# Performance work log

Hardware: AMD Instinct MI355X
Metric: run time of the kernel (lower is better)

The kernel has to match this reference:

```python
import jax, jax.numpy as jnp
import numpy as np

MIN_LOGITS_VALUE = -2.3819763e+38
MAX_WAVELENGTH = 10000


def _apply_rope(inputs, positions):
    # inputs: [b, t, n, h]; positions: [b, t]. RoPE on first half of h.
    x_rope, x = jnp.split(inputs, 2, axis=-1)
    pos = positions[:, :, None, None].astype(jnp.float32)  # [b, t, 1, 1]
    freq_exponents = 2.0 * jnp.arange(x_rope.shape[-1] // 2) / x_rope.shape[-1]
    inv_freq = 1.0 / (MAX_WAVELENGTH ** freq_exponents)
    sinusoid = pos * inv_freq  # [b, t, 1, h/2]
    sin = jnp.sin(sinusoid).astype(inputs.dtype)
    cos = jnp.cos(sinusoid).astype(inputs.dtype)
    first, second = jnp.split(x_rope, 2, axis=-1)
    return jnp.concatenate(
        [first * cos - second * sin, second * cos + first * sin, x], axis=-1)


def _forward_pass_mask(segment_pos, window_size):
    # segment_pos: [b, t]; 0 marks a segment start.
    segment_ids = jnp.cumsum(segment_pos == 0, axis=-1)  # [b, t]
    t = segment_pos.shape[-1]
    positions = jnp.arange(t)
    same_segment = segment_ids[:, :, None] == segment_ids[:, None, :]
    causal = positions[:, None] >= positions[None, :]
    window = positions[:, None] <= positions[None, :] + window_size
    return same_segment & (causal & window)[None]  # [b, t, t]


def setup_inputs() -> dict:
    key = jax.random.key(0)
    ks = jax.random.split(key, 6)
    B, T, W, N = 2, 2048, 2048, 16
    H = W // N
    x = jax.random.normal(ks[0], (B, T, W), jnp.float32)
    sc = 1.0 / np.sqrt(W).astype(np.float32)
    w_q = jax.random.normal(ks[1], (W, W), jnp.float32) * sc
    w_k = jax.random.normal(ks[2], (W, H), jnp.float32) * sc
    w_v = jax.random.normal(ks[3], (W, H), jnp.float32) * sc
    w_out = jax.random.normal(ks[4], (W, W), jnp.float32) * sc
    b_out = jnp.zeros((W,), jnp.float32)
    segment_pos = jnp.tile(jnp.arange(T, dtype=jnp.int32)[None], (B, 1))
    return {"x": x, "w_q": w_q, "w_k": w_k, "w_v": w_v, "w_out": w_out,
            "b_out": b_out, "segment_pos": segment_pos,
            "num_heads": N, "window_size": 1024}


def reference(x, w_q, w_k, w_v, w_out, b_out, segment_pos, num_heads, window_size):
    b, t, width = x.shape
    head_dim = width // num_heads
    # Projections: MQA -> keys/values are single-head [b, t, head_dim].
    q = (x @ w_q).reshape(b, t, num_heads, head_dim)
    k = (x @ w_k)[:, :, None, :]  # [b, t, 1, h]
    v = x @ w_v                   # [b, t, h]
    q = _apply_rope(q, segment_pos)
    k = _apply_rope(k, segment_pos)[:, :, 0]  # [b, t, h]
    logits = jnp.einsum('btnh,bsh->bnts', q, k) * (head_dim ** -0.5)
    mask = _forward_pass_mask(segment_pos, window_size)  # [b, t, t]
    masked = jnp.where(mask[:, None], logits, MIN_LOGITS_VALUE).astype(jnp.float32)
    probs = jax.nn.softmax(masked, axis=-1).astype(x.dtype)
    encoded = jnp.einsum('bnts,bsh->btnh', probs, v).reshape(b, t, width)
    return encoded @ w_out + b_out
```

## Files before the change

kernel.cpp:

```cpp
#include <hip/hip_runtime.h>
#include <hip/hip_bf16.h>
#include <stdint.h>

typedef __attribute__((ext_vector_type(8))) short short8;
typedef __attribute__((ext_vector_type(4))) float f32x4;

__device__ __forceinline__ float bf2f(short u) {
  return __uint_as_float(((unsigned)(unsigned short)u) << 16);
}
__device__ __forceinline__ short f2bf(float f) {
  unsigned x = __float_as_uint(f);
  unsigned r = (x + 0x7fffu + ((x >> 16) & 1u)) >> 16;
  return (short)r;
}

__device__ __forceinline__ void gload_lds16(const short* g, short* l) {
  __builtin_amdgcn_global_load_lds(
      (const __attribute__((address_space(1))) void*)g,
      (__attribute__((address_space(3))) void*)l, 16, 0, 0);
}

__global__ void cast_x_bf16(const float* __restrict__ in, short* __restrict__ out, int n8) {
  int i = blockIdx.x * blockDim.x + threadIdx.x;
  if (i >= n8) return;
  const float4* p = (const float4*)in + (size_t)i * 2;
  float4 a = p[0], b = p[1];
  short8 o;
  o[0] = f2bf(a.x); o[1] = f2bf(a.y); o[2] = f2bf(a.z); o[3] = f2bf(a.w);
  o[4] = f2bf(b.x); o[5] = f2bf(b.y); o[6] = f2bf(b.z); o[7] = f2bf(b.w);
  *((short8*)out + i) = o;
}

__global__ void transpose_cast(const float* __restrict__ in, int R, int C,
                               short* __restrict__ out, int row_off, int ldo) {
  __shared__ float tile[32][33];
  int c0 = blockIdx.x * 32, r0 = blockIdx.y * 32;
  int tx = threadIdx.x, ty = threadIdx.y;
#pragma unroll
  for (int i = 0; i < 4; ++i)
    tile[ty + i * 8][tx] = in[(size_t)(r0 + ty + i * 8) * C + (c0 + tx)];
  __syncthreads();
#pragma unroll
  for (int i = 0; i < 4; ++i)
    out[(size_t)(row_off + c0 + ty + i * 8) * ldo + (r0 + tx)] =
        f2bf(tile[tx][ty + i * 8]);
}

__global__ void transpose_v(const short* __restrict__ qkv, short* __restrict__ vT,
                            int T, int LD, int vcol) {
  __shared__ short tile[32][33];
  int t0 = blockIdx.x * 32, h0 = blockIdx.y * 32, b = blockIdx.z;
  int tx = threadIdx.x, ty = threadIdx.y;
#pragma unroll
  for (int i = 0; i < 4; ++i)
    tile[ty + i * 8][tx] = qkv[((size_t)b * T + t0 + ty + i * 8) * LD + vcol + h0 + tx];
  __syncthreads();
#pragma unroll
  for (int i = 0; i < 4; ++i)
    vT[((size_t)b * 128 + h0 + ty + i * 8) * T + t0 + tx] = tile[tx][ty + i * 8];
}

template <int OUT_F32>
__global__ __launch_bounds__(512, 2)
void gemm256(const short* __restrict__ A, const short* __restrict__ Bt,
             int M, int N, int K, int ldc,
             short* __restrict__ outb, float* __restrict__ outf,
             const float* __restrict__ bias) {
  __shared__ short As[2][256 * 64];
  __shared__ short Bs[2][256 * 64];
  const int tid = threadIdx.x, lane = tid & 63, w = tid >> 6;
  const int wm = w >> 2, wn = w & 3;
  const int l15 = lane & 15, l4 = lane >> 4;
  const int m0 = blockIdx.y * 256, n0 = blockIdx.x * 256;
  const int sw = (l15 & 7) << 4;
  const int NT = K / 64;

  f32x4 acc[8][4] = {};
  short8 a[4][2], b[4][2];

  auto stage = [&](short* dst, const short* src, int base0, int k0) {
#pragma unroll
    for (int i = 0; i < 4; ++i) {
      int chunk = i * 8 + w;
      int r = chunk * 8 + (lane >> 3);
      int cs = ((lane & 7) ^ ((lane >> 3) & 7)) * 8;
      gload_lds16(src + (size_t)(base0 + r) * K + k0 + cs, dst + chunk * 512);
    }
  };

  auto rdA = [&](const short* buf, int mi, int kk) -> short8 {
    int row = wm * 128 + mi * 16 + l15;
    int byt = row * 128 + ((kk * 64 + l4 * 16) ^ sw);
    return *(const short8*)((const char*)buf + byt);
  };
  auto rdB = [&](const short* buf, int ni, int kk) -> short8 {
    int row = wn * 64 + ni * 16 + l15;
    int byt = row * 128 + ((kk * 64 + l4 * 16) ^ sw);
    return *(const short8*)((const char*)buf + byt);
  };

  stage(As[0], A, m0, 0);
  stage(Bs[0], Bt, n0, 0);
  asm volatile("s_waitcnt vmcnt(0)" ::: "memory");
  __builtin_amdgcn_s_barrier();

  for (int t = 0; t < NT; ++t) {
    const int bf = t & 1, nb = bf ^ 1;
    const bool pre = (t + 1 < NT);
    const short* Ab = As[bf];
    const short* Bb = Bs[bf];

#pragma unroll
    for (int mg = 0; mg < 4; ++mg) { a[mg][0] = rdA(Ab, mg, 0); a[mg][1] = rdA(Ab, mg, 1); }
#pragma unroll
    for (int ng = 0; ng < 2; ++ng) { b[ng][0] = rdB(Bb, ng, 0); b[ng][1] = rdB(Bb, ng, 1); }
    if (pre) stage(As[nb], A, m0, (t + 1) * 64);
    __builtin_amdgcn_s_barrier();
    __builtin_amdgcn_s_setprio(1);
#pragma unroll
    for (int mg = 0; mg < 4; ++mg)
#pragma unroll
      for (int ng = 0; ng < 2; ++ng) {
        acc[mg][ng] = __builtin_amdgcn_mfma_f32_16x16x32_bf16(a[mg][0], b[ng][0], acc[mg][ng], 0, 0, 0);
        acc[mg][ng] = __builtin_amdgcn_mfma_f32_16x16x32_bf16(a[mg][1], b[ng][1], acc[mg][ng], 0, 0, 0);
      }
    __builtin_amdgcn_s_setprio(0);
    __builtin_amdgcn_s_barrier();

#pragma unroll
    for (int ng = 2; ng < 4; ++ng) { b[ng][0] = rdB(Bb, ng, 0); b[ng][1] = rdB(Bb, ng, 1); }
    if (pre) stage(Bs[nb], Bt, n0, (t + 1) * 64);
    __builtin_amdgcn_s_barrier();
    __builtin_amdgcn_s_setprio(1);
#pragma unroll
    for (int mg = 0; mg < 4; ++mg)
#pragma unroll
      for (int ng = 2; ng < 4; ++ng) {
        acc[mg][ng] = __builtin_amdgcn_mfma_f32_16x16x32_bf16(a[mg][0], b[ng][0], acc[mg][ng], 0, 0, 0);
        acc[mg][ng] = __builtin_amdgcn_mfma_f32_16x16x32_bf16(a[mg][1], b[ng][1], acc[mg][ng], 0, 0, 0);
      }
    __builtin_amdgcn_s_setprio(0);
    __builtin_amdgcn_s_barrier();

#pragma unroll
    for (int mg = 0; mg < 4; ++mg) { a[mg][0] = rdA(Ab, mg + 4, 0); a[mg][1] = rdA(Ab, mg + 4, 1); }
    __builtin_amdgcn_s_barrier();
    __builtin_amdgcn_s_setprio(1);
#pragma unroll
    for (int mg = 0; mg < 4; ++mg)
#pragma unroll
      for (int ng = 0; ng < 2; ++ng) {
        acc[mg + 4][ng] = __builtin_amdgcn_mfma_f32_16x16x32_bf16(a[mg][0], b[ng][0], acc[mg + 4][ng], 0, 0, 0);
        acc[mg + 4][ng] = __builtin_amdgcn_mfma_f32_16x16x32_bf16(a[mg][1], b[ng][1], acc[mg + 4][ng], 0, 0, 0);
      }
    __builtin_amdgcn_s_setprio(0);
    __builtin_amdgcn_s_barrier();

    __builtin_amdgcn_s_setprio(1);
#pragma unroll
    for (int mg = 0; mg < 4; ++mg)
#pragma unroll
      for (int ng = 2; ng < 4; ++ng) {
        acc[mg + 4][ng] = __builtin_amdgcn_mfma_f32_16x16x32_bf16(a[mg][0], b[ng][0], acc[mg + 4][ng], 0, 0, 0);
        acc[mg + 4][ng] = __builtin_amdgcn_mfma_f32_16x16x32_bf16(a[mg][1], b[ng][1], acc[mg + 4][ng], 0, 0, 0);
      }
    __builtin_amdgcn_s_setprio(0);
    asm volatile("s_waitcnt vmcnt(0)" ::: "memory");
    __builtin_amdgcn_s_barrier();
  }

#pragma unroll
  for (int mi = 0; mi < 8; ++mi)
#pragma unroll
    for (int ni = 0; ni < 4; ++ni)
#pragma unroll
      for (int r = 0; r < 4; ++r) {
        int row = m0 + wm * 128 + mi * 16 + l4 * 4 + r;
        int col = n0 + wn * 64 + ni * 16 + l15;
        if (OUT_F32)
          outf[(size_t)row * ldc + col] = acc[mi][ni][r] + bias[col];
        else
          outb[(size_t)row * ldc + col] = f2bf(acc[mi][ni][r]);
      }
}

__global__ void rope_kernel(short* __restrict__ qkv, const int* __restrict__ segpos,
                            int nheads, int hd, int ld) {
  const int row = blockIdx.x;
  const float pos = (float)segpos[row];
  short* base = qkv + (size_t)row * ld;
  const int quarter = hd >> 2;
  const int npairs_q = nheads * quarter;
  const int total = npairs_q + quarter;
  for (int p = threadIdx.x; p < total; p += blockDim.x) {
    int i, off;
    if (p < npairs_q) { off = (p >> 5) * hd; i = p & 31; }
    else              { off = nheads * hd;  i = p - npairs_q; }
    float ang = pos * exp2f(-(float)i * (13.287712379549449f / (float)quarter));
    float s, c;
    sincosf(ang, &s, &c);
    float a = bf2f(base[off + i]);
    float b = bf2f(base[off + quarter + i]);
    base[off + i]           = f2bf(a * c - b * s);
    base[off + quarter + i] = f2bf(b * c + a * s);
  }
}

__global__ __launch_bounds__(512)
void attn_kernel(const short* __restrict__ qkv, const short* __restrict__ vT,
                 short* __restrict__ enc,
                 const int* __restrict__ wsz_p, int T, int nheads, int nqt, int bhc) {
  const int window = wsz_p[0];
  const int i = blockIdx.x;
  const int qt = nqt - 1 - (i / bhc);
  const int bh = i % bhc;
  const int b = bh / nheads, n = bh % nheads;
  const int tid = threadIdx.x, lane = tid & 63, w = tid >> 6;
  const int l15 = lane & 15, l4 = lane >> 4;
  const int q0 = qt * 128;
  const size_t rowbase = (size_t)b * T;
  const int LD = nheads * 128 + 256;
  const int kcol = nheads * 128;
  const float CC = 0.08838834764831845f * 1.4426950408889634f;

  __shared__ short Ks[64 * 128];
  __shared__ short Vt[128 * 64];
  __shared__ short Pl[8][16 * 72];

  short8 qf[4];
  {
    const short* qptr = qkv + (rowbase + q0 + w * 16 + l15) * LD + n * 128 + l4 * 8;
#pragma unroll
    for (int kk = 0; kk < 4; ++kk) qf[kk] = *(const short8*)(qptr + kk * 32);
  }
  f32x4 o[8] = {};
  float mrow[4], lrow[4];
#pragma unroll
  for (int r = 0; r < 4; ++r) { mrow[r] = -1e30f; lrow[r] = 0.f; }

  const int tmin = q0 + w * 16, tmax = tmin + 15;
  int st_lo = q0 - window; if (st_lo < 0) st_lo = 0; st_lo >>= 6;
  const int st_hi = (q0 + 127) >> 6;

  short8 kreg[2], vreg[2];
  auto load_tile = [&](int s0) {
#pragma unroll
    for (int it = 0; it < 2; ++it) {
      int c = it * 512 + tid;
      kreg[it] = *(const short8*)(qkv + (rowbase + s0 + (c >> 4)) * (size_t)LD + kcol + (c & 15) * 8);
      vreg[it] = *(const short8*)(vT + ((size_t)b * 128 + (c >> 3)) * T + s0 + (c & 7) * 8);
    }
  };
  auto store_tile = [&]() {
#pragma unroll
    for (int it = 0; it < 2; ++it) {
      int c = it * 512 + tid;
      int r = c >> 4;
      *(short8*)((char*)Ks + ((r * 256 + (c & 15) * 16) ^ ((r & 7) << 4))) = kreg[it];
      int h = c >> 3;
      *(short8*)((char*)Vt + ((h * 128 + (c & 7) * 16) ^ ((h & 7) << 4))) = vreg[it];
    }
  };

  load_tile(st_lo * 64);
  store_tile();
  __syncthreads();

  for (int st = st_lo; st <= st_hi; ++st) {
    const int s0 = st * 64;
    const bool more = (st < st_hi);
    if (more) load_tile(s0 + 64);

    const bool active = (s0 <= tmax) && (tmin <= s0 + 63 + window);
    if (active) {
      f32x4 sacc[4];
      __builtin_amdgcn_s_setprio(1);
#pragma unroll
      for (int si = 0; si < 4; ++si) {
        f32x4 acc = {};
        int srow = si * 16 + l15;
#pragma unroll
        for (int kk = 0; kk < 4; ++kk) {
          int byt = (srow * 256 + (kk * 32 + l4 * 8) * 2) ^ ((srow & 7) << 4);
          short8 kf = *(const short8*)((const char*)Ks + byt);
          acc = __builtin_amdgcn_mfma_f32_16x16x32_bf16(qf[kk], kf, acc, 0, 0, 0);
        }
        sacc[si] = acc;
      }
      __builtin_amdgcn_s_setprio(0);

      const int trow0 = q0 + w * 16 + l4 * 4;
      const bool full = (s0 + 63 <= tmin) && (tmax <= s0 + window);
      float mt[4];
      if (full) {
#pragma unroll
        for (int r = 0; r < 4; ++r)
          mt[r] = fmaxf(fmaxf(sacc[0][r], sacc[1][r]), fmaxf(sacc[2][r], sacc[3][r]));
      } else {
#pragma unroll
        for (int r = 0; r < 4; ++r) mt[r] = -1e30f;
#pragma unroll
        for (int si = 0; si < 4; ++si) {
          int s = s0 + si * 16 + l15;
#pragma unroll
          for (int r = 0; r < 4; ++r) {
            int t = trow0 + r;
            float v = (s <= t && t <= s + window) ? sacc[si][r] : -1e30f;
            sacc[si][r] = v;
            mt[r] = fmaxf(mt[r], v);
          }
        }
      }
#pragma unroll
      for (int r = 0; r < 4; ++r)
#pragma unroll
        for (int off = 1; off < 16; off <<= 1)
          mt[r] = fmaxf(mt[r], __shfl_xor(mt[r], off));

      bool dfr = true;
#pragma unroll
      for (int r = 0; r < 4; ++r) dfr = dfr && ((mt[r] - mrow[r]) * CC <= 8.0f);
      const bool defer = __all(dfr);
      float fac[4];
      if (!defer) {
#pragma unroll
        for (int r = 0; r < 4; ++r) {
          float mnew = fmaxf(mrow[r], mt[r]);
          fac[r] = exp2f((mrow[r] - mnew) * CC);
          mrow[r] = mnew;
        }
      }
      float psum[4];
#pragma unroll
      for (int r = 0; r < 4; ++r) psum[r] = 0.f;
#pragma unroll
      for (int si = 0; si < 4; ++si)
#pragma unroll
        for (int r = 0; r < 4; ++r) {
          float p = exp2f((sacc[si][r] - mrow[r]) * CC);
          psum[r] += p;
          Pl[w][(l4 * 4 + r) * 72 + si * 16 + l15] = f2bf(p);
        }
#pragma unroll
      for (int r = 0; r < 4; ++r) {
#pragma unroll
        for (int off = 1; off < 16; off <<= 1)
          psum[r] += __shfl_xor(psum[r], off);
        if (!defer) lrow[r] = lrow[r] * fac[r] + psum[r];
        else        lrow[r] += psum[r];
      }
      if (!defer) {
#pragma unroll
        for (int nt = 0; nt < 8; ++nt)
#pragma unroll
          for (int r = 0; r < 4; ++r) o[nt][r] *= fac[r];
      }

      __builtin_amdgcn_s_setprio(1);
#pragma unroll
      for (int kk = 0; kk < 2; ++kk) {
        short8 pf = *(const short8*)(&Pl[w][l15 * 72 + kk * 32 + l4 * 8]);
#pragma unroll
        for (int nt = 0; nt < 8; ++nt) {
          int h = nt * 16 + l15;
          int vb = (h * 128 + kk * 64 + l4 * 16) ^ ((h & 7) << 4);
          short8 vf = *(const short8*)((const char*)Vt + vb);
          o[nt] = __builtin_amdgcn_mfma_f32_16x16x32_bf16(pf, vf, o[nt], 0, 0, 0);
        }
      }
      __builtin_amdgcn_s_setprio(0);
    }
    __syncthreads();
    if (more) store_tile();
    __syncthreads();
  }

#pragma unroll
  for (int nt = 0; nt < 8; ++nt)
#pragma unroll
    for (int r = 0; r < 4; ++r) {
      size_t row = rowbase + q0 + w * 16 + l4 * 4 + r;
      int col = n * 128 + nt * 16 + l15;
      enc[row * (size_t)(nheads * 128) + col] = f2bf(o[nt][r] / lrow[r]);
    }
}

extern "C" void kernel_launch(void* const* d_in, const int* in_sizes, int n_in,
                              void* d_out, int out_size, void* d_ws, size_t ws_size,
                              hipStream_t stream) {
  const float* x     = (const float*)d_in[0];
  const float* w_q   = (const float*)d_in[1];
  const float* w_k   = (const float*)d_in[2];
  const float* w_v   = (const float*)d_in[3];
  const float* w_out = (const float*)d_in[4];
  const float* b_out = (const float*)d_in[5];
  const int* segpos  = (const int*)d_in[6];
  const int* wsz     = (const int*)d_in[8];
  float* out = (float*)d_out;

  const int BT = in_sizes[6];
  const int W  = in_sizes[5];
  const int H  = in_sizes[2] / W;
  const int NH = W / H;
  const int T  = 2048;
  const int B  = BT / T;
  const int NQKV = W + 2 * H;

  char* ws = (char*)d_ws;
  short* xb    = (short*)ws;
  short* wqkvT = (short*)(ws + (size_t)BT * W * 2);
  short* woutT = (short*)(ws + (size_t)(BT * W + NQKV * W) * 2);
  short* qkv   = (short*)(ws + (size_t)(BT * W + NQKV * W + W * W) * 2);
  short* vTp   = wqkvT;
  short* enc   = xb;

  int n8 = BT * W / 8;
  cast_x_bf16<<<(n8 + 255) / 256, 256, 0, stream>>>(x, xb, n8);

  dim3 tb(32, 8);
  transpose_cast<<<dim3(W / 32, W / 32), tb, 0, stream>>>(w_q, W, W, wqkvT, 0, W);
  transpose_cast<<<dim3(H / 32, W / 32), tb, 0, stream>>>(w_k, W, H, wqkvT, W, W);
  transpose_cast<<<dim3(H / 32, W / 32), tb, 0, stream>>>(w_v, W, H, wqkvT, W + H, W);
  transpose_cast<<<dim3(W / 32, W / 32), tb, 0, stream>>>(w_out, W, W, woutT, 0, W);

  gemm256<0><<<dim3(NQKV / 256, BT / 256), 512, 0, stream>>>(
      xb, wqkvT, BT, NQKV, W, NQKV, qkv, nullptr, nullptr);

  rope_kernel<<<BT, 256, 0, stream>>>(qkv, segpos, NH, H, NQKV);

  transpose_v<<<dim3(T / 32, H / 32, B), tb, 0, stream>>>(qkv, vTp, T, NQKV, NH * H + H);

  const int nqt = T / 128;
  const int bhc = B * NH;
  attn_kernel<<<nqt * bhc, 512, 0, stream>>>(qkv, vTp, enc, wsz, T, NH, nqt, bhc);

  gemm256<1><<<dim3(W / 256, BT / 256), 512, 0, stream>>>(
      enc, woutT, BT, W, W, W, nullptr, out, b_out);
}
```

Measured before the change: 359.0 us.

## Replace double-buffered GEMM with four-slot K=32 ring pipeline

Rewrites the bf16 GEMM main loop to use a four-slot shared-memory ring of K=32 tiles, prefetching two steps ahead with partial vmcnt waits and a single barrier per iteration. It also changes the LDS swizzle to a 4-chunk XOR pattern. The aim is to cut the many barriers per K-step and hide global-load latency better. In exchange there are twice as many loop iterations, smaller MFMA batches per barrier, and a new swizzle that may cause LDS bank conflicts. The ring also relies on waitcnt accounting being correct for the global_load_lds ops.

After: 403.8 us. +12.5%, slower.

```diff
diff --git a/kernel.cpp b/kernel.cpp
--- a/kernel.cpp
+++ b/kernel.cpp
@@ -62,110 +62,62 @@
 
 template <int OUT_F32>
 __global__ __launch_bounds__(512, 2)
-void gemm256(const short* __restrict__ A, const short* __restrict__ Bt,
-             int M, int N, int K, int ldc,
-             short* __restrict__ outb, float* __restrict__ outf,
-             const float* __restrict__ bias) {
-  __shared__ short As[2][256 * 64];
-  __shared__ short Bs[2][256 * 64];
+void gemm_ring(const short* __restrict__ A, const short* __restrict__ Bt,
+               int M, int N, int K, int ldc,
+               short* __restrict__ outb, float* __restrict__ outf,
+               const float* __restrict__ bias) {
+  __shared__ short As[4][256 * 32];
+  __shared__ short Bs[4][256 * 32];
   const int tid = threadIdx.x, lane = tid & 63, w = tid >> 6;
   const int wm = w >> 2, wn = w & 3;
   const int l15 = lane & 15, l4 = lane >> 4;
   const int m0 = blockIdx.y * 256, n0 = blockIdx.x * 256;
-  const int sw = (l15 & 7) << 4;
-  const int NT = K / 64;
+  const int NT = K / 32;
+  const int cswz = (l4 ^ ((l15 >> 1) & 3)) * 8;
 
   f32x4 acc[8][4] = {};
-  short8 a[4][2], b[4][2];
-
-  auto stage = [&](short* dst, const short* src, int base0, int k0) {
-#pragma unroll
-    for (int i = 0; i < 4; ++i) {
-      int chunk = i * 8 + w;
-      int r = chunk * 8 + (lane >> 3);
-      int cs = ((lane & 7) ^ ((lane >> 3) & 7)) * 8;
-      gload_lds16(src + (size_t)(base0 + r) * K + k0 + cs, dst + chunk * 512);
-    }
-  };
-
-  auto rdA = [&](const short* buf, int mi, int kk) -> short8 {
-    int row = wm * 128 + mi * 16 + l15;
-    int byt = row * 128 + ((kk * 64 + l4 * 16) ^ sw);
-    return *(const short8*)((const char*)buf + byt);
-  };
-  auto rdB = [&](const short* buf, int ni, int kk) -> short8 {
-    int row = wn * 64 + ni * 16 + l15;
-    int byt = row * 128 + ((kk * 64 + l4 * 16) ^ sw);
-    return *(const short8*)((const char*)buf + byt);
+
+  auto stage = [&](short* dst, const short* src, int base0, int kt) {
+#pragma unroll
+    for (int i = 0; i < 2; ++i) {
+      int ci = tid + 512 * i;
+      int r = ci >> 2, s = ci & 3;
+      int gs = s ^ ((r >> 1) & 3);
+      gload_lds16(src + (size_t)(base0 + r) * K + kt * 32 + gs * 8, dst + ci * 8);
+    }
   };
 
   stage(As[0], A, m0, 0);
   stage(Bs[0], Bt, n0, 0);
-  asm volatile("s_waitcnt vmcnt(0)" ::: "memory");
+  stage(As[1], A, m0, 1);
+  stage(Bs[1], Bt, n0, 1);
+  asm volatile("s_waitcnt vmcnt(4)" ::: "memory");
   __builtin_amdgcn_s_barrier();
 
+#pragma unroll 4
   for (int t = 0; t < NT; ++t) {
-    const int bf = t & 1, nb = bf ^ 1;
-    const bool pre = (t + 1 < NT);
-    const short* Ab = As[bf];
-    const short* Bb = Bs[bf];
-
-#pragma unroll
-    for (int mg = 0; mg < 4; ++mg) { a[mg][0] = rdA(Ab, mg, 0); a[mg][1] = rdA(Ab, mg, 1); }
-#pragma unroll
-    for (int ng = 0; ng < 2; ++ng) { b[ng][0] = rdB(Bb, ng, 0); b[ng][1] = rdB(Bb, ng, 1); }
-    if (pre) stage(As[nb], A, m0, (t + 1) * 64);
-    __builtin_amdgcn_s_barrier();
+    const int slot = t & 3;
+    const bool pre = (t + 2 < NT);
+    if (pre) {
+      stage(As[(t + 2) & 3], A, m0, t + 2);
+      stage(Bs[(t + 2) & 3], Bt, n0, t + 2);
+    }
+    short8 af[8], bf[4];
+#pragma unroll
+    for (int mi = 0; mi < 8; ++mi)
+      af[mi] = *(const short8*)(As[slot] + (wm * 128 + mi * 16 + l15) * 32 + cswz);
+#pragma unroll
+    for (int ni = 0; ni < 4; ++ni)
+      bf[ni] = *(const short8*)(Bs[slot] + (wn * 64 + ni * 16 + l15) * 32 + cswz);
     __builtin_amdgcn_s_setprio(1);
 #pragma unroll
-    for (int mg = 0; mg < 4; ++mg)
-#pragma unroll
-      for (int ng = 0; ng < 2; ++ng) {
-        acc[mg][ng] = __builtin_amdgcn_mfma_f32_16x16x32_bf16(a[mg][0], b[ng][0], acc[mg][ng], 0, 0, 0);
-        acc[mg][ng] = __builtin_amdgcn_mfma_f32_16x16x32_bf16(a[mg][1], b[ng][1], acc[mg][ng], 0, 0, 0);
-      }
+    for (int mi = 0; mi < 8; ++mi)
+#pragma unroll
+      for (int ni = 0; ni < 4; ++ni)
+        acc[mi][ni] = __builtin_amdgcn_mfma_f32_16x16x32_bf16(af[mi], bf[ni], acc[mi][ni], 0, 0, 0);
     __builtin_amdgcn_s_setprio(0);
-    __builtin_amdgcn_s_barrier();
-
-#pragma unroll
-    for (int ng = 2; ng < 4; ++ng) { b[ng][0] = rdB(Bb, ng, 0); b[ng][1] = rdB(Bb, ng, 1); }
-    if (pre) stage(Bs[nb], Bt, n0, (t + 1) * 64);
-    __builtin_amdgcn_s_barrier();
-    __builtin_amdgcn_s_setprio(1);
-#pragma unroll
-    for (int mg = 0; mg < 4; ++mg)
-#pragma unroll
-      for (int ng = 2; ng < 4; ++ng) {
-        acc[mg][ng] = __builtin_amdgcn_mfma_f32_16x16x32_bf16(a[mg][0], b[ng][0], acc[mg][ng], 0, 0, 0);
-        acc[mg][ng] = __builtin_amdgcn_mfma_f32_16x16x32_bf16(a[mg][1], b[ng][1], acc[mg][ng], 0, 0, 0);
-      }
-    __builtin_amdgcn_s_setprio(0);
-    __builtin_amdgcn_s_barrier();
-
-#pragma unroll
-    for (int mg = 0; mg < 4; ++mg) { a[mg][0] = rdA(Ab, mg + 4, 0); a[mg][1] = rdA(Ab, mg + 4, 1); }
-    __builtin_amdgcn_s_barrier();
-    __builtin_amdgcn_s_setprio(1);
-#pragma unroll
-    for (int mg = 0; mg < 4; ++mg)
-#pragma unroll
-      for (int ng = 0; ng < 2; ++ng) {
-        acc[mg + 4][ng] = __builtin_amdgcn_mfma_f32_16x16x32_bf16(a[mg][0], b[ng][0], acc[mg + 4][ng], 0, 0, 0);
-        acc[mg + 4][ng] = __builtin_amdgcn_mfma_f32_16x16x32_bf16(a[mg][1], b[ng][1], acc[mg + 4][ng], 0, 0, 0);
-      }
-    __builtin_amdgcn_s_setprio(0);
-    __builtin_amdgcn_s_barrier();
-
-    __builtin_amdgcn_s_setprio(1);
-#pragma unroll
-    for (int mg = 0; mg < 4; ++mg)
-#pragma unroll
-      for (int ng = 2; ng < 4; ++ng) {
-        acc[mg + 4][ng] = __builtin_amdgcn_mfma_f32_16x16x32_bf16(a[mg][0], b[ng][0], acc[mg + 4][ng], 0, 0, 0);
-        acc[mg + 4][ng] = __builtin_amdgcn_mfma_f32_16x16x32_bf16(a[mg][1], b[ng][1], acc[mg + 4][ng], 0, 0, 0);
-      }
-    __builtin_amdgcn_s_setprio(0);
-    asm volatile("s_waitcnt vmcnt(0)" ::: "memory");
+    if (pre) asm volatile("s_waitcnt vmcnt(4)" ::: "memory");
+    else     asm volatile("s_waitcnt vmcnt(0)" ::: "memory");
     __builtin_amdgcn_s_barrier();
   }
 
@@ -423,7 +375,7 @@
   transpose_cast<<<dim3(H / 32, W / 32), tb, 0, stream>>>(w_v, W, H, wqkvT, W + H, W);
   transpose_cast<<<dim3(W / 32, W / 32), tb, 0, stream>>>(w_out, W, W, woutT, 0, W);
 
-  gemm256<0><<<dim3(NQKV / 256, BT / 256), 512, 0, stream>>>(
+  gemm_ring<0><<<dim3(NQKV / 256, BT / 256), 512, 0, stream>>>(
       xb, wqkvT, BT, NQKV, W, NQKV, qkv, nullptr, nullptr);
 
   rope_kernel<<<BT, 256, 0, stream>>>(qkv, segpos, NH, H, NQKV);
@@ -434,6 +386,6 @@
   const int bhc = B * NH;
   attn_kernel<<<nqt * bhc, 512, 0, stream>>>(qkv, vTp, enc, wsz, T, NH, nqt, bhc);
 
-  gemm256<1><<<dim3(W / 256, BT / 256), 512, 0, stream>>>(
+  gemm_ring<1><<<dim3(W / 256, BT / 256), 512, 0, stream>>>(
       enc, woutT, BT, W, W, W, nullptr, out, b_out);
 }
```
